# Optimization experiments

Measured on AMD Instinct MI355X. Metric: run time of the kernel, lower is better.

Reference implementation:

```python
import jax, jax.numpy as jnp
import numpy as np

N_CODES = 8192
EMBED_DIM = 64
N_VOXELS = 32768


def setup_inputs() -> dict:
    key = jax.random.key(0)
    k1, k2 = jax.random.split(key)
    z_feats = jax.random.normal(k1, (N_VOXELS, EMBED_DIM), dtype=jnp.float32)
    embeddings = jax.random.normal(k2, (N_CODES, EMBED_DIM), dtype=jnp.float32)
    return {"z_feats": z_feats, "embeddings": embeddings}


def reference(z_feats, embeddings):
    # Pairwise squared euclidean distances: ||z||^2 - 2 z.e + ||e||^2  [N, K]
    z_sq = jnp.sum(z_feats * z_feats, axis=1, keepdims=True)        # [N, 1]
    e_sq = jnp.sum(embeddings * embeddings, axis=1)[None, :]        # [1, K]
    d2 = z_sq - 2.0 * jnp.einsum('nd,kd->nk', z_feats, embeddings) + e_sq
    # argmin is invariant under sqrt (cdist returns sqrt, but only indices are used)
    encoding_indices = jnp.argmin(d2, axis=1)                        # [N]
    quantized_feats = embeddings[encoding_indices]                   # [N, D]
    # commitment_loss = mse(z, sg(q));  vq_loss = mse(q, sg(z)) (gradient mode)
    commitment_loss = jnp.mean((z_feats - jax.lax.stop_gradient(quantized_feats)) ** 2)
    vq_loss = jnp.mean((quantized_feats - jax.lax.stop_gradient(z_feats)) ** 2)
    # straight-through estimator
    quantized_st = z_feats + jax.lax.stop_gradient(quantized_feats - z_feats)
    indices_out = encoding_indices[:, None].astype(jnp.float32)      # [N, 1]
    return quantized_st, vq_loss, commitment_loss, indices_out
```

## Files before the change

kernel.cpp:

```cpp
#include <hip/hip_runtime.h>
#include <float.h>

#define N_VOX 32768
#define N_CODES 8192
#define DIM 64

#define Q_OFF 0
#define VQ_OFF (N_VOX * DIM)
#define CM_OFF (VQ_OFF + 1)
#define IDX_OFF (VQ_OFF + 2)

#define WS_ACC 0
#define WS_CNT 1
#define WS_ESQH 64
#define WS_IDX (WS_ESQH + N_CODES)
#define WS_EHI (WS_IDX + N_VOX)
#define WS_ELO (WS_EHI + N_CODES * DIM / 2)

typedef _Float16 half8 __attribute__((ext_vector_type(8)));
typedef float floatx4 __attribute__((ext_vector_type(4)));

__device__ inline void gld16(const void* g, void* l) {
  __builtin_amdgcn_global_load_lds(
      (const __attribute__((address_space(1))) unsigned int*)g,
      (__attribute__((address_space(3))) unsigned int*)l, 16, 0, 0);
}
__device__ inline void gld4(const void* g, void* l) {
  __builtin_amdgcn_global_load_lds(
      (const __attribute__((address_space(1))) unsigned int*)g,
      (__attribute__((address_space(3))) unsigned int*)l, 4, 0, 0);
}

__global__ __launch_bounds__(256) void k_cvt(const float* __restrict__ e,
                                             float* __restrict__ ws) {
  int gid = blockIdx.x * 256 + threadIdx.x;
  if (gid == 0) {
    ws[WS_ACC] = 0.f;
    ((int*)ws)[WS_CNT] = 0;
  }
  int row = gid >> 3, c = gid & 7;
  const float* src = e + (size_t)row * DIM + c * 8;
  float4 a = *(const float4*)src;
  float4 b = *(const float4*)(src + 4);
  float x[8] = {a.x, a.y, a.z, a.w, b.x, b.y, b.z, b.w};
  float s = 0.f;
  half8 hv, lv;
  #pragma unroll
  for (int j = 0; j < 8; ++j) {
    s += x[j] * x[j];
    _Float16 h = (_Float16)x[j];
    hv[j] = h;
    lv[j] = (_Float16)(x[j] - (float)h);
  }
  s += __shfl_xor(s, 1); s += __shfl_xor(s, 2); s += __shfl_xor(s, 4);
  if (c == 0) ws[WS_ESQH + row] = 0.5f * s;
  int p = (c + row) & 7;
  ((half8*)(ws + WS_EHI))[row * 8 + p] = hv;
  ((half8*)(ws + WS_ELO))[row * 8 + p] = lv;
}

__global__ __launch_bounds__(256, 2) void k_argmin(const float* __restrict__ z,
                                                   const float* __restrict__ e,
                                                   float* __restrict__ ws,
                                                   float* __restrict__ out) {
  __shared__ __align__(16) _Float16 sBhi[2][128 * 64];
  __shared__ __align__(16) _Float16 sBlo[2][128 * 64];
  __shared__ float sEsq[2][128];
  __shared__ float sMval[128];
  __shared__ int   sMidx[128];
  __shared__ int   sWin[64];
  __shared__ float sWsum[4];

  const int tid  = threadIdx.x;
  const int lane = tid & 63;
  const int wave = tid >> 6;
  const int n16  = lane & 15;
  const int quad = lane >> 4;
  const int vgrp = wave >> 1;
  const int chalf = wave & 1;
  const int vb = blockIdx.x * 64;

  const char* ehi_b = (const char*)(ws + WS_EHI);
  const char* elo_b = (const char*)(ws + WS_ELO);
  const char* esq_b = (const char*)(ws + WS_ESQH);

  half8 ahi[2][2], alo[2][2];
  #pragma unroll
  for (int m = 0; m < 2; ++m)
    #pragma unroll
    for (int kc = 0; kc < 2; ++kc) {
      const float* src = z + (size_t)(vb + vgrp * 32 + m * 16 + n16) * DIM
                       + kc * 32 + quad * 8;
      float4 a = *(const float4*)src;
      float4 b = *(const float4*)(src + 4);
      float x[8] = {a.x, a.y, a.z, a.w, b.x, b.y, b.z, b.w};
      #pragma unroll
      for (int j = 0; j < 8; ++j) {
        _Float16 h = (_Float16)x[j];
        ahi[m][kc][j] = h;
        alo[m][kc][j] = (_Float16)(x[j] - (float)h);
      }
    }

  float bval[2][4]; int bidx[2][4];
  #pragma unroll
  for (int m = 0; m < 2; ++m)
    #pragma unroll
    for (int r = 0; r < 4; ++r) { bval[m][r] = FLT_MAX; bidx[m][r] = 0; }

  const int s0 = ((quad + n16) & 7) * 8;
  const int s1 = ((quad + 4 + n16) & 7) * 8;

  auto stage = [&](int buf, int ct) {
    const size_t cbb = (size_t)ct * 128 * 128;
    #pragma unroll
    for (int r = 0; r < 4; ++r) {
      int off = (r * 4 + wave) * 1024;
      gld16(ehi_b + cbb + off + lane * 16, (char*)sBhi[buf] + off);
      gld16(elo_b + cbb + off + lane * 16, (char*)sBlo[buf] + off);
    }
    if (wave == 0) {
      gld4(esq_b + (size_t)ct * 512 + lane * 4, (char*)sEsq[buf]);
      gld4(esq_b + (size_t)ct * 512 + 256 + lane * 4, (char*)sEsq[buf] + 256);
    }
  };

  stage(0, 0);
  __syncthreads();

  for (int ct = 0; ct < 64; ++ct) {
    const int cur = ct & 1;
    if (ct < 63) stage(cur ^ 1, ct + 1);

    const _Float16* bhiP = sBhi[cur];
    const _Float16* bloP = sBlo[cur];
    const float*    esqP = sEsq[cur];
    const int cb = ct * 128;

    #pragma unroll
    for (int t = 0; t < 4; ++t) {
      const int row = chalf * 64 + t * 16 + n16;
      half8 bh0 = *(const half8*)&bhiP[row * 64 + s0];
      half8 bh1 = *(const half8*)&bhiP[row * 64 + s1];
      half8 bl0 = *(const half8*)&bloP[row * 64 + s0];
      half8 bl1 = *(const half8*)&bloP[row * 64 + s1];
      float eh = esqP[row];
      int code = cb + row;
      #pragma unroll
      for (int m = 0; m < 2; ++m) {
        floatx4 acc = {0.f, 0.f, 0.f, 0.f};
        acc = __builtin_amdgcn_mfma_f32_16x16x32_f16(ahi[m][0], bh0, acc, 0, 0, 0);
        acc = __builtin_amdgcn_mfma_f32_16x16x32_f16(ahi[m][1], bh1, acc, 0, 0, 0);
        acc = __builtin_amdgcn_mfma_f32_16x16x32_f16(ahi[m][0], bl0, acc, 0, 0, 0);
        acc = __builtin_amdgcn_mfma_f32_16x16x32_f16(ahi[m][1], bl1, acc, 0, 0, 0);
        acc = __builtin_amdgcn_mfma_f32_16x16x32_f16(alo[m][0], bh0, acc, 0, 0, 0);
        acc = __builtin_amdgcn_mfma_f32_16x16x32_f16(alo[m][1], bh1, acc, 0, 0, 0);
        #pragma unroll
        for (int r = 0; r < 4; ++r) {
          float tv = eh - acc[r];
          if (tv < bval[m][r]) { bval[m][r] = tv; bidx[m][r] = code; }
        }
      }
    }
    __syncthreads();
  }

  #pragma unroll
  for (int m = 0; m < 2; ++m)
    #pragma unroll
    for (int r = 0; r < 4; ++r) {
      float v = bval[m][r]; int i = bidx[m][r];
      #pragma unroll
      for (int off = 1; off < 16; off <<= 1) {
        float ov = __shfl_xor(v, off);
        int   oi = __shfl_xor(i, off);
        if (ov < v || (ov == v && oi < i)) { v = ov; i = oi; }
      }
      if (n16 == 0) {
        int vox = vgrp * 32 + m * 16 + quad * 4 + r;
        sMval[chalf * 64 + vox] = v;
        sMidx[chalf * 64 + vox] = i;
      }
    }
  __syncthreads();

  if (tid < 64) {
    float v0 = sMval[tid], v1 = sMval[64 + tid];
    int   i0 = sMidx[tid], i1 = sMidx[64 + tid];
    bool p1 = (v1 < v0) || (v1 == v0 && i1 < i0);
    int w = p1 ? i1 : i0;
    sWin[tid] = w;
    out[IDX_OFF + vb + tid] = (float)w;
  }
  __syncthreads();

  {
    const int vox = tid >> 2;
    const int dc = (tid & 3) * 16;
    const int gi = sWin[vox];
    const float* er = e + (size_t)gi * DIM + dc;
    const float* zr = z + (size_t)(vb + vox) * DIM + dc;
    float* qr = out + Q_OFF + (size_t)(vb + vox) * DIM + dc;
    float local = 0.f;
    #pragma unroll
    for (int j = 0; j < 4; ++j) {
      float4 e4 = *(const float4*)(er + j * 4);
      float4 z4 = *(const float4*)(zr + j * 4);
      *(float4*)(qr + j * 4) = e4;
      float dx = z4.x - e4.x, dy = z4.y - e4.y, dz = z4.z - e4.z, dw = z4.w - e4.w;
      local += dx * dx + dy * dy + dz * dz + dw * dw;
    }
    #pragma unroll
    for (int off = 32; off; off >>= 1) local += __shfl_xor(local, off);
    if ((tid & 63) == 0) sWsum[wave] = local;
    __syncthreads();
    if (tid == 0) {
      float bs = sWsum[0] + sWsum[1] + sWsum[2] + sWsum[3];
      atomicAdd(ws + WS_ACC, bs);
      __threadfence();
      int done = atomicAdd((int*)ws + WS_CNT, 1);
      if (done == (int)gridDim.x - 1) {
        float s = atomicAdd(ws + WS_ACC, 0.f);
        float mv = s * (1.0f / (float)(N_VOX * DIM));
        out[VQ_OFF] = mv;
        out[CM_OFF] = mv;
      }
    }
  }
}

extern "C" void kernel_launch(void* const* d_in, const int* in_sizes, int n_in,
                              void* d_out, int out_size, void* d_ws, size_t ws_size,
                              hipStream_t stream) {
  const float* z = (const float*)d_in[0];
  const float* e = (const float*)d_in[1];
  float* out = (float*)d_out;
  float* ws = (float*)d_ws;

  k_cvt<<<(N_CODES * 8) / 256, 256, 0, stream>>>(e, ws);
  k_argmin<<<N_VOX / 64, 256, 0, stream>>>(z, e, ws, out);
}
```

Measured before the change: 189.3 us.

## Give each wave all 64 voxels, fold bias into MFMA accumulator, split acc chains

Each wave now holds A fragments for all 64 voxels and handles 32 codes per tile, instead of 32 voxels by 64 codes. That halves the LDS reads of B per MFMA and raises register use. The negated half-norm seeds the accumulator, so the argmin becomes an argmax and the per-element subtraction goes away. Two independent accumulator chains shorten MFMA dependency latency, s_setprio raises priority during the MFMA burst, and the final cross-wave reduction now merges four partials.

Result: slower. 199.7 us (+5.5%).

```diff
diff --git a/kernel.cpp b/kernel.cpp
--- a/kernel.cpp
+++ b/kernel.cpp
@@ -29,6 +29,10 @@
   __builtin_amdgcn_global_load_lds(
       (const __attribute__((address_space(1))) unsigned int*)g,
       (__attribute__((address_space(3))) unsigned int*)l, 4, 0, 0);
+}
+
+__device__ __forceinline__ floatx4 mfma16(half8 a, half8 b, floatx4 c) {
+  return __builtin_amdgcn_mfma_f32_16x16x32_f16(a, b, c, 0, 0, 0);
 }
 
 __global__ __launch_bounds__(256) void k_cvt(const float* __restrict__ e,
@@ -53,7 +57,7 @@
     lv[j] = (_Float16)(x[j] - (float)h);
   }
   s += __shfl_xor(s, 1); s += __shfl_xor(s, 2); s += __shfl_xor(s, 4);
-  if (c == 0) ws[WS_ESQH + row] = 0.5f * s;
+  if (c == 0) ws[WS_ESQH + row] = -0.5f * s;
   int p = (c + row) & 7;
   ((half8*)(ws + WS_EHI))[row * 8 + p] = hv;
   ((half8*)(ws + WS_ELO))[row * 8 + p] = lv;
@@ -66,8 +70,8 @@
   __shared__ __align__(16) _Float16 sBhi[2][128 * 64];
   __shared__ __align__(16) _Float16 sBlo[2][128 * 64];
   __shared__ float sEsq[2][128];
-  __shared__ float sMval[128];
-  __shared__ int   sMidx[128];
+  __shared__ float sMval[4][64];
+  __shared__ int   sMidx[4][64];
   __shared__ int   sWin[64];
   __shared__ float sWsum[4];
 
@@ -76,20 +80,18 @@
   const int wave = tid >> 6;
   const int n16  = lane & 15;
   const int quad = lane >> 4;
-  const int vgrp = wave >> 1;
-  const int chalf = wave & 1;
   const int vb = blockIdx.x * 64;
 
   const char* ehi_b = (const char*)(ws + WS_EHI);
   const char* elo_b = (const char*)(ws + WS_ELO);
   const char* esq_b = (const char*)(ws + WS_ESQH);
 
-  half8 ahi[2][2], alo[2][2];
-  #pragma unroll
-  for (int m = 0; m < 2; ++m)
+  half8 ahi[4][2], alo[4][2];
+  #pragma unroll
+  for (int m = 0; m < 4; ++m)
     #pragma unroll
     for (int kc = 0; kc < 2; ++kc) {
-      const float* src = z + (size_t)(vb + vgrp * 32 + m * 16 + n16) * DIM
+      const float* src = z + (size_t)(vb + m * 16 + n16) * DIM
                        + kc * 32 + quad * 8;
       float4 a = *(const float4*)src;
       float4 b = *(const float4*)(src + 4);
@@ -102,11 +104,11 @@
       }
     }
 
-  float bval[2][4]; int bidx[2][4];
-  #pragma unroll
-  for (int m = 0; m < 2; ++m)
-    #pragma unroll
-    for (int r = 0; r < 4; ++r) { bval[m][r] = FLT_MAX; bidx[m][r] = 0; }
+  float bmax[4][4]; int bidx[4][4];
+  #pragma unroll
+  for (int m = 0; m < 4; ++m)
+    #pragma unroll
+    for (int r = 0; r < 4; ++r) { bmax[m][r] = -FLT_MAX; bidx[m][r] = 0; }
 
   const int s0 = ((quad + n16) & 7) * 8;
   const int s1 = ((quad + 4 + n16) & 7) * 8;
@@ -135,62 +137,66 @@
     const _Float16* bhiP = sBhi[cur];
     const _Float16* bloP = sBlo[cur];
     const float*    esqP = sEsq[cur];
-    const int cb = ct * 128;
-
-    #pragma unroll
-    for (int t = 0; t < 4; ++t) {
-      const int row = chalf * 64 + t * 16 + n16;
+    const int cbase = ct * 128;
+
+    #pragma unroll
+    for (int t = 0; t < 2; ++t) {
+      const int row = wave * 32 + t * 16 + n16;
       half8 bh0 = *(const half8*)&bhiP[row * 64 + s0];
       half8 bh1 = *(const half8*)&bhiP[row * 64 + s1];
       half8 bl0 = *(const half8*)&bloP[row * 64 + s0];
       half8 bl1 = *(const half8*)&bloP[row * 64 + s1];
-      float eh = esqP[row];
-      int code = cb + row;
+      float nh = esqP[row];
+      int code = cbase + row;
+      __builtin_amdgcn_s_setprio(1);
       #pragma unroll
-      for (int m = 0; m < 2; ++m) {
-        floatx4 acc = {0.f, 0.f, 0.f, 0.f};
-        acc = __builtin_amdgcn_mfma_f32_16x16x32_f16(ahi[m][0], bh0, acc, 0, 0, 0);
-        acc = __builtin_amdgcn_mfma_f32_16x16x32_f16(ahi[m][1], bh1, acc, 0, 0, 0);
-        acc = __builtin_amdgcn_mfma_f32_16x16x32_f16(ahi[m][0], bl0, acc, 0, 0, 0);
-        acc = __builtin_amdgcn_mfma_f32_16x16x32_f16(ahi[m][1], bl1, acc, 0, 0, 0);
-        acc = __builtin_amdgcn_mfma_f32_16x16x32_f16(alo[m][0], bh0, acc, 0, 0, 0);
-        acc = __builtin_amdgcn_mfma_f32_16x16x32_f16(alo[m][1], bh1, acc, 0, 0, 0);
+      for (int m = 0; m < 4; ++m) {
+        floatx4 acc0 = {nh, nh, nh, nh};
+        floatx4 acc1 = {0.f, 0.f, 0.f, 0.f};
+        acc0 = mfma16(ahi[m][0], bh0, acc0);
+        acc1 = mfma16(ahi[m][1], bh1, acc1);
+        acc0 = mfma16(ahi[m][0], bl0, acc0);
+        acc1 = mfma16(ahi[m][1], bl1, acc1);
+        acc0 = mfma16(alo[m][0], bh0, acc0);
+        acc1 = mfma16(alo[m][1], bh1, acc1);
         #pragma unroll
         for (int r = 0; r < 4; ++r) {
-          float tv = eh - acc[r];
-          if (tv < bval[m][r]) { bval[m][r] = tv; bidx[m][r] = code; }
+          float tv = acc0[r] + acc1[r];
+          if (tv > bmax[m][r]) { bmax[m][r] = tv; bidx[m][r] = code; }
         }
       }
+      __builtin_amdgcn_s_setprio(0);
     }
     __syncthreads();
   }
 
   #pragma unroll
-  for (int m = 0; m < 2; ++m)
+  for (int m = 0; m < 4; ++m)
     #pragma unroll
     for (int r = 0; r < 4; ++r) {
-      float v = bval[m][r]; int i = bidx[m][r];
+      float v = bmax[m][r]; int i = bidx[m][r];
       #pragma unroll
       for (int off = 1; off < 16; off <<= 1) {
         float ov = __shfl_xor(v, off);
         int   oi = __shfl_xor(i, off);
-        if (ov < v || (ov == v && oi < i)) { v = ov; i = oi; }
+        if (ov > v || (ov == v && oi < i)) { v = ov; i = oi; }
       }
       if (n16 == 0) {
-        int vox = vgrp * 32 + m * 16 + quad * 4 + r;
-        sMval[chalf * 64 + vox] = v;
-        sMidx[chalf * 64 + vox] = i;
+        sMval[wave][m * 16 + quad * 4 + r] = v;
+        sMidx[wave][m * 16 + quad * 4 + r] = i;
       }
     }
   __syncthreads();
 
   if (tid < 64) {
-    float v0 = sMval[tid], v1 = sMval[64 + tid];
-    int   i0 = sMidx[tid], i1 = sMidx[64 + tid];
-    bool p1 = (v1 < v0) || (v1 == v0 && i1 < i0);
-    int w = p1 ? i1 : i0;
-    sWin[tid] = w;
-    out[IDX_OFF + vb + tid] = (float)w;
+    float v = sMval[0][tid]; int i = sMidx[0][tid];
+    #pragma unroll
+    for (int q = 1; q < 4; ++q) {
+      float ov = sMval[q][tid]; int oi = sMidx[q][tid];
+      if (ov > v || (ov == v && oi < i)) { v = ov; i = oi; }
+    }
+    sWin[tid] = i;
+    out[IDX_OFF + vb + tid] = (float)i;
   }
   __syncthreads();
 
```
